# Kernel optimization log

Hardware: AMD Instinct MI355X
Metric: run time of the kernel (lower is better)

The kernel has to match this reference:

```python
import jax, jax.numpy as jnp
import numpy as np

N_WIRES = 6
DIM = 1 << N_WIRES  # 64, equals input channel dim C for amplitude encoding
HID = N_WIRES       # hidden_dim = len(ops)


def _rx(theta):
    c = jnp.cos(theta / 2).astype(jnp.complex64)
    s = jnp.sin(theta / 2).astype(jnp.complex64)
    return jnp.stack([jnp.stack([c, -1j * s]), jnp.stack([-1j * s, c])])


def _ry(theta):
    c = jnp.cos(theta / 2).astype(jnp.complex64)
    s = jnp.sin(theta / 2).astype(jnp.complex64)
    return jnp.stack([jnp.stack([c, -s]), jnp.stack([s, c])])


def _apply_1q(state, U, wire):
    # state: (N, 2, 2, ..., 2); apply 2x2 U on qubit axis wire+1
    s = jnp.moveaxis(state, wire + 1, 1)
    s = jnp.einsum('ab,nb...->na...', U, s)
    return jnp.moveaxis(s, 1, wire + 1)


def _apply_cnot(state, c, t):
    # flip target axis where control bit == 1
    s = jnp.moveaxis(state, (c + 1, t + 1), (1, 2))
    s = jnp.concatenate([s[:, :1], jnp.flip(s[:, 1:2], axis=2)], axis=1)
    return jnp.moveaxis(s, (1, 2), (c + 1, t + 1))


def _expval_z(state, wire):
    # <Z_wire> = P(bit=0) - P(bit=1)
    p = state.real ** 2 + state.imag ** 2
    p = jnp.moveaxis(p, wire + 1, 1).reshape(p.shape[0], 2, -1)
    return p[:, 0].sum(-1) - p[:, 1].sum(-1)


def _value_layer(x_flat, params, qk):
    # amplitude encoding: normalize input into state amplitudes (C == DIM)
    norm = jnp.linalg.norm(x_flat, axis=-1, keepdims=True)
    psi = (x_flat / norm).astype(jnp.complex64)
    state = psi.reshape((x_flat.shape[0],) + (2,) * N_WIRES)
    rx0, ry0, ry1 = params[0], params[1], params[2]
    for j in range(N_WIRES):
        state = _apply_1q(state, _rx(rx0[j]), j)
        state = _apply_1q(state, _ry(ry0[j]), j)
    for j in range(N_WIRES):
        state = _apply_cnot(state, j, (j + 1) % N_WIRES)
    for j in range(N_WIRES):
        state = _apply_1q(state, _ry(ry1[j]), j)
    if qk:
        z0 = _expval_z(state, 0)
        return jnp.stack([z0] * HID, axis=-1)  # qk=True replicates wire-0 <Z>
    return jnp.stack([_expval_z(state, w) for w in range(N_WIRES)], axis=-1)


def setup_inputs() -> dict:
    key = jax.random.key(0)
    k1, k2, k3, k4 = jax.random.split(key, 4)
    B, T, C = 16, 2048, DIM
    return {
        'x': jax.random.normal(k1, (B, T, C), dtype=jnp.float32),
        'params_q': jax.random.normal(k2, (3, N_WIRES), dtype=jnp.float32),
        'params_k': jax.random.normal(k3, (3, N_WIRES), dtype=jnp.float32),
        'params_v': jax.random.normal(k4, (3, N_WIRES), dtype=jnp.float32),
    }


def reference(x, params_q, params_k, params_v):
    B, T, C = x.shape
    xf = x.reshape(B * T, C)
    q = _value_layer(xf, params_q, True).reshape(B, T, HID)
    k = _value_layer(xf, params_k, True).reshape(B, T, HID)
    v = _value_layer(xf, params_v, False).reshape(B, T, HID)
    scores = jnp.einsum('btd,bsd->bts', q, k) / jnp.sqrt(jnp.float32(HID))
    attn = jax.nn.softmax(scores, axis=-1)
    return jnp.einsum('bts,bsd->btd', attn, v)
```

## Files before the change

### kernel.cpp

```cpp
#include <hip/hip_runtime.h>
#include <math.h>

#define NWIRES 6
#define DIM 64
#define NTOK 32768
#define NBATCH 16
#define TPB 2048
#define NMOM 16
#define SQRT6F 2.4494897427831781f
#define APAD 76

typedef short bf16x8 __attribute__((ext_vector_type(8)));
typedef float f32x4  __attribute__((ext_vector_type(4)));

__device__ __forceinline__ unsigned f2bfbits(float f) {
    unsigned u = __float_as_uint(f);
    return (u + 0x7FFF + ((u >> 16) & 1)) >> 16;
}
__device__ __forceinline__ float bfbits2f(unsigned b) {
    return __uint_as_float(b << 16);
}
__device__ __forceinline__ float pswap(float v) { return __shfl_xor(v, 1, 64); }

__global__ __attribute__((amdgpu_waves_per_eu(1, 4)))
__launch_bounds__(256) void qsa_sim(
        const float* __restrict__ x,
        const float* __restrict__ pq,
        const float* __restrict__ pk,
        const float* __restrict__ pv,
        float* __restrict__ zq,
        float* __restrict__ kv) {
    __shared__ unsigned short sAh[128 * APAD];
    __shared__ unsigned short sAl[128 * APAD];
    __shared__ float sTc[64], sTs[64], sP[24];
    int tid = threadIdx.x;
    int tbase = blockIdx.x * 256;
    int circ = blockIdx.y;
    const float* p = (circ == 0) ? pq : (circ == 1 ? pk : pv);

    int lane = tid & 63, wv = tid >> 6;
    int q4 = lane >> 4, c16 = lane & 15;
    float4 rw[8];
#pragma unroll
    for (int cg = 0; cg < 2; ++cg) {
        const float* xr = x + ((size_t)(tbase + wv * 64 + cg * 16 + c16)) * 64;
#pragma unroll
        for (int ks = 0; ks < 2; ++ks) {
            rw[cg * 4 + ks * 2 + 0] = *(const float4*)(xr + ks * 32 + q4 * 8);
            rw[cg * 4 + ks * 2 + 1] = *(const float4*)(xr + ks * 32 + q4 * 8 + 4);
        }
    }

    if (tid < 64) {
        int b = tid;
        float d = 0.f;
#pragma unroll
        for (int j = 0; j < 6; ++j)
            d += 0.5f * p[j] * ((b & (32 >> j)) ? -1.f : 1.f);
        float sd, cd;
        sincosf(d, &sd, &cd);
        sTc[b] = cd;
        sTs[b] = sd;
        if (b < 12) {
            float s, cc;
            sincosf(0.5f * p[6 + b], &s, &cc);
            sP[b * 2 + 0] = cc;
            sP[b * 2 + 1] = s;
        }
    }
    __syncthreads();

    {
        int ph = tid >> 7;
        int k  = (tid >> 1) & 63;
        int h  = tid & 1;
        const float* sTx = ph ? sTs : sTc;
        float v[32];
#pragma unroll
        for (int i = 0; i < 32; ++i) {
            int g = h * 32 + i;
            v[i] = (__popc(g & k) & 1) ? -sTx[g] : sTx[g];
        }
#pragma unroll
        for (int i = 0; i < 32; ++i) {
            float pv_ = pswap(v[i]);
            v[i] = h ? (pv_ - v[i]) : (v[i] + pv_);
        }
#pragma unroll
        for (int M = 16; M >= 1; M >>= 1) {
#pragma unroll
            for (int i = 0; i < 32; ++i) {
                if (i & M) continue;
                int j = i | M;
                float a = v[i], b = v[j];
                v[i] = a + b; v[j] = a - b;
            }
        }
#pragma unroll
        for (int layer = 0; layer < 2; ++layer) {
            const float* Pl = sP + layer * 12;
            {
                float c = Pl[0], ss = h ? Pl[1] : -Pl[1];
#pragma unroll
                for (int i = 0; i < 32; ++i) {
                    float pv_ = pswap(v[i]);
                    v[i] = c * v[i] + ss * pv_;
                }
            }
#pragma unroll
            for (int w = 1; w < 6; ++w) {
                int M = 32 >> w;
                float c = Pl[w * 2], s = Pl[w * 2 + 1];
#pragma unroll
                for (int i = 0; i < 32; ++i) {
                    if (i & M) continue;
                    int j = i | M;
                    float a = v[i], b = v[j];
                    v[i] = c * a - s * b;
                    v[j] = s * a + c * b;
                }
            }
            if (layer == 0) {
#pragma unroll
                for (int i = 0; i < 16; ++i) {
                    int j = i | 16;
                    float a = v[i], b = v[j];
                    v[i] = h ? b : a;
                    v[j] = h ? a : b;
                }
#pragma unroll
                for (int w = 1; w < 5; ++w) {
                    int MC = 32 >> w, MT = MC >> 1;
#pragma unroll
                    for (int i = 0; i < 32; ++i) {
                        if (!(i & MC) || (i & MT)) continue;
                        int j = i | MT;
                        float t = v[i]; v[i] = v[j]; v[j] = t;
                    }
                }
#pragma unroll
                for (int i = 1; i < 32; i += 2) v[i] = pswap(v[i]);
            }
        }
#pragma unroll
        for (int i = 0; i < 32; ++i) {
            int row = ph * 64 + h * 32 + i;
            unsigned hb = f2bfbits(v[i]);
            unsigned lb = f2bfbits(v[i] - bfbits2f(hb));
            sAh[row * APAD + k] = (unsigned short)hb;
            sAl[row * APAD + k] = (unsigned short)lb;
        }
    }
    __syncthreads();

    bf16x8 xh[2][2], xl[2][2];
#pragma unroll 1
    for (int pr = 0; pr < 2; ++pr) {
#pragma unroll
        for (int cg = 0; cg < 2; ++cg) {
#pragma unroll
            for (int ks = 0; ks < 2; ++ks) {
                float4 f0 = rw[cg * 4 + ks * 2], f1 = rw[cg * 4 + ks * 2 + 1];
                float ff[8] = {f0.x, f0.y, f0.z, f0.w, f1.x, f1.y, f1.z, f1.w};
#pragma unroll
                for (int e = 0; e < 8; ++e) {
                    unsigned hb = f2bfbits(ff[e]);
                    unsigned lb = f2bfbits(ff[e] - bfbits2f(hb));
                    xh[cg][ks][e] = (short)hb;
                    xl[cg][ks][e] = (short)lb;
                }
            }
        }
        if (pr == 0) {
#pragma unroll
            for (int cg = 0; cg < 2; ++cg) {
                const float* xr = x + ((size_t)(tbase + wv * 64 + (2 + cg) * 16 + c16)) * 64;
#pragma unroll
                for (int ks = 0; ks < 2; ++ks) {
                    rw[cg * 4 + ks * 2 + 0] = *(const float4*)(xr + ks * 32 + q4 * 8);
                    rw[cg * 4 + ks * 2 + 1] = *(const float4*)(xr + ks * 32 + q4 * 8 + 4);
                }
            }
        }

        f32x4 acc[2][8];
#pragma unroll
        for (int cg = 0; cg < 2; ++cg)
#pragma unroll
            for (int mt = 0; mt < 8; ++mt) acc[cg][mt] = (f32x4){0.f, 0.f, 0.f, 0.f};

#pragma unroll
        for (int mt = 0; mt < 8; ++mt) {
            int r = mt * 16 + c16;
#pragma unroll
            for (int ks = 0; ks < 2; ++ks) {
                const uint2* ph_ = (const uint2*)(&sAh[r * APAD + ks * 32 + q4 * 8]);
                const uint2* pl_ = (const uint2*)(&sAl[r * APAD + ks * 32 + q4 * 8]);
                union { uint2 u[2]; bf16x8 v; } ua, ub;
                ua.u[0] = ph_[0]; ua.u[1] = ph_[1];
                ub.u[0] = pl_[0]; ub.u[1] = pl_[1];
                bf16x8 ah = ua.v, al = ub.v;
#pragma unroll
                for (int cg = 0; cg < 2; ++cg) {
                    acc[cg][mt] = __builtin_amdgcn_mfma_f32_16x16x32_bf16(ah, xh[cg][ks], acc[cg][mt], 0, 0, 0);
                    acc[cg][mt] = __builtin_amdgcn_mfma_f32_16x16x32_bf16(ah, xl[cg][ks], acc[cg][mt], 0, 0, 0);
                    acc[cg][mt] = __builtin_amdgcn_mfma_f32_16x16x32_bf16(al, xh[cg][ks], acc[cg][mt], 0, 0, 0);
                }
            }
        }

#pragma unroll
        for (int cg = 0; cg < 2; ++cg) {
            float n = 0.f, s0 = 0.f, s1 = 0.f, s2 = 0.f, s3 = 0.f, s4 = 0.f, s5 = 0.f;
            float f2 = (q4 < 2) ? 1.f : 0.f;
            float f3 = (q4 & 1) ? 0.f : 1.f;
#pragma unroll
            for (int mt = 0; mt < 4; ++mt) {
#pragma unroll
                for (int rg = 0; rg < 4; ++rg) {
                    float dc = acc[cg][mt][rg];
                    float ds = acc[cg][mt + 4][rg];
                    float pp = dc * dc + ds * ds;
                    n += pp;
                    if (!(mt & 2)) s0 += pp;
                    if (!(mt & 1)) s1 += pp;
                    s2 += f2 * pp;
                    s3 += f3 * pp;
                    if (!(rg & 2)) s4 += pp;
                    if (!(rg & 1)) s5 += pp;
                }
            }
#pragma unroll
            for (int d = 16; d <= 32; d <<= 1) {
                n  += __shfl_xor(n,  d, 64);
                s0 += __shfl_xor(s0, d, 64);
                s1 += __shfl_xor(s1, d, 64);
                s2 += __shfl_xor(s2, d, 64);
                s3 += __shfl_xor(s3, d, 64);
                s4 += __shfl_xor(s4, d, 64);
                s5 += __shfl_xor(s5, d, 64);
            }
            if (q4 == 0) {
                int t = tbase + wv * 64 + (pr * 2 + cg) * 16 + c16;
                float inv = 1.0f / n;
                if (circ == 0) {
                    zq[t] = SQRT6F * (2.f * s0 - n) * inv;
                } else if (circ == 1) {
                    kv[(size_t)t * 8] = (2.f * s0 - n) * inv;
                } else {
                    float* o = kv + (size_t)t * 8;
                    o[1] = (2.f*s0 - n) * inv;
                    o[2] = (2.f*s1 - n) * inv;
                    o[3] = (2.f*s2 - n) * inv;
                    o[4] = (2.f*s3 - n) * inv;
                    o[5] = (2.f*s4 - n) * inv;
                    o[6] = (2.f*s5 - n) * inv;
                    o[7] = 0.f;
                }
            }
        }
    }
}

__global__ __attribute__((amdgpu_waves_per_eu(1, 2)))
__launch_bounds__(64) void qsa_moments_partial(
        const float* __restrict__ kv,
        float* __restrict__ mpart) {
    __shared__ float sm[64 * 113];
    int blk = blockIdx.x;
    int b = blk >> 3, c = blk & 7;
    int lane = threadIdx.x;
    float S[NMOM], H[NMOM][6];
#pragma unroll
    for (int m = 0; m < NMOM; ++m) {
        S[m] = 0.f;
#pragma unroll
        for (int w = 0; w < 6; ++w) H[m][w] = 0.f;
    }
    const float* base = kv + ((size_t)(b * TPB + c * 256)) * 8;
#pragma unroll
    for (int r = 0; r < 4; ++r) {
        const float4* e = (const float4*)(base + (size_t)(r * 64 + lane) * 8);
        float4 e0 = e[0], e1 = e[1];
        float z = e0.x;
        float v0 = e0.y, v1 = e0.z, v2 = e0.w, v3 = e1.x, v4 = e1.y, v5 = e1.z;
        float pw = 1.f;
#pragma unroll
        for (int m = 0; m < NMOM; ++m) {
            S[m] += pw;
            H[m][0] += pw * v0; H[m][1] += pw * v1; H[m][2] += pw * v2;
            H[m][3] += pw * v3; H[m][4] += pw * v4; H[m][5] += pw * v5;
            pw *= z;
        }
    }
    float* row = sm + lane * 113;
#pragma unroll
    for (int m = 0; m < NMOM; ++m) {
        row[m * 7 + 0] = S[m];
        row[m * 7 + 1] = H[m][0]; row[m * 7 + 2] = H[m][1];
        row[m * 7 + 3] = H[m][2]; row[m * 7 + 4] = H[m][3];
        row[m * 7 + 5] = H[m][4]; row[m * 7 + 6] = H[m][5];
    }
    __syncthreads();
#pragma unroll
    for (int vbase = 0; vbase < 2; ++vbase) {
        int v = vbase * 64 + lane;
        if (v < 112) {
            float s = 0.f;
#pragma unroll
            for (int r = 0; r < 64; ++r) s += sm[r * 113 + v];
            mpart[(size_t)blk * 112 + v] = s;
        }
    }
}

__global__ __launch_bounds__(256) void qsa_eval(
        const float* __restrict__ zq,
        const float* __restrict__ mpart,
        float* __restrict__ out) {
    __shared__ float sm[112];
    int bk = blockIdx.x;
    int b = bk >> 3;
    int tid = threadIdx.x;
    if (tid < 112) {
        float s = 0.f;
#pragma unroll
        for (int c = 0; c < 8; ++c) s += mpart[(size_t)(b * 8 + c) * 112 + tid];
        sm[tid] = s;
    }
    __syncthreads();

    int t = bk * 256 + tid;
    float a = zq[t];
    float den = 0.f, o0 = 0.f, o1 = 0.f, o2 = 0.f, o3 = 0.f, o4 = 0.f, o5 = 0.f;
    float pw = 1.f;
#pragma unroll
    for (int m = 0; m < NMOM; ++m) {
        const float* mm = sm + m * 7;
        den += pw * mm[0];
        o0 += pw * mm[1]; o1 += pw * mm[2]; o2 += pw * mm[3];
        o3 += pw * mm[4]; o4 += pw * mm[5]; o5 += pw * mm[6];
        pw *= a * (1.0f / (m + 1));
    }
    float inv = 1.0f / den;
    float* o = out + (size_t)t * 6;
    float2* o2p = (float2*)o;
    o2p[0] = make_float2(o0 * inv, o1 * inv);
    o2p[1] = make_float2(o2 * inv, o3 * inv);
    o2p[2] = make_float2(o4 * inv, o5 * inv);
}

extern "C" void kernel_launch(void* const* d_in, const int* in_sizes, int n_in,
                              void* d_out, int out_size, void* d_ws, size_t ws_size,
                              hipStream_t stream) {
    const float* x  = (const float*)d_in[0];
    const float* pq = (const float*)d_in[1];
    const float* pk = (const float*)d_in[2];
    const float* pv = (const float*)d_in[3];
    float* w = (float*)d_ws;
    float* zq    = w;
    float* kv    = zq + NTOK;
    float* mpart = kv + NTOK * 8;
    float* out   = (float*)d_out;

    qsa_sim<<<dim3(NTOK / 256, 3), 256, 0, stream>>>(x, pq, pk, pv, zq, kv);
    qsa_moments_partial<<<NBATCH * 8, 64, 0, stream>>>(kv, mpart);
    qsa_eval<<<NTOK / 256, 256, 0, stream>>>(zq, mpart, out);
}
```

Measured before the change: 88.48 us.

## Fuse moment reduction into simulation kernel and share x tiles across K/V

The separate moments kernel and the global kv intermediate buffer are removed. Each block of the second grid row now builds unitaries for both the K and V circuits, evaluates both on the same x registers, and stages z and v expectations in LDS. It then computes the per-block power moments there and writes mpart directly. This saves one kernel launch, a global write and read of the kv buffer, and one of the three passes over x. In exchange the K/V blocks carry twice the work of the Q blocks, and LDS use per block roughly doubles, which may lower occupancy.

```diff
diff --git a/kernel.cpp b/kernel.cpp
--- a/kernel.cpp
+++ b/kernel.cpp
@@ -9,6 +9,7 @@
 #define NMOM 16
 #define SQRT6F 2.4494897427831781f
 #define APAD 76
+#define ZP 260
 
 typedef short bf16x8 __attribute__((ext_vector_type(8)));
 typedef float f32x4  __attribute__((ext_vector_type(4)));
@@ -22,35 +23,10 @@
 }
 __device__ __forceinline__ float pswap(float v) { return __shfl_xor(v, 1, 64); }
 
-__global__ __attribute__((amdgpu_waves_per_eu(1, 4)))
-__launch_bounds__(256) void qsa_sim(
-        const float* __restrict__ x,
-        const float* __restrict__ pq,
-        const float* __restrict__ pk,
-        const float* __restrict__ pv,
-        float* __restrict__ zq,
-        float* __restrict__ kv) {
-    __shared__ unsigned short sAh[128 * APAD];
-    __shared__ unsigned short sAl[128 * APAD];
-    __shared__ float sTc[64], sTs[64], sP[24];
-    int tid = threadIdx.x;
-    int tbase = blockIdx.x * 256;
-    int circ = blockIdx.y;
-    const float* p = (circ == 0) ? pq : (circ == 1 ? pk : pv);
-
-    int lane = tid & 63, wv = tid >> 6;
-    int q4 = lane >> 4, c16 = lane & 15;
-    float4 rw[8];
-#pragma unroll
-    for (int cg = 0; cg < 2; ++cg) {
-        const float* xr = x + ((size_t)(tbase + wv * 64 + cg * 16 + c16)) * 64;
-#pragma unroll
-        for (int ks = 0; ks < 2; ++ks) {
-            rw[cg * 4 + ks * 2 + 0] = *(const float4*)(xr + ks * 32 + q4 * 8);
-            rw[cg * 4 + ks * 2 + 1] = *(const float4*)(xr + ks * 32 + q4 * 8 + 4);
-        }
-    }
-
+
+__device__ __forceinline__ void build_A(const float* __restrict__ p,
+        unsigned short* sAh, unsigned short* sAl,
+        float* sTc, float* sTs, float* sP, int tid) {
     if (tid < 64) {
         int b = tid;
         float d = 0.f;
@@ -152,6 +128,48 @@
         }
     }
     __syncthreads();
+}
+
+__global__ __attribute__((amdgpu_waves_per_eu(1, 4)))
+__launch_bounds__(256) void qsa_sim(
+        const float* __restrict__ x,
+        const float* __restrict__ pq,
+        const float* __restrict__ pk,
+        const float* __restrict__ pv,
+        float* __restrict__ zq,
+        float* __restrict__ mpart) {
+    __shared__ __align__(16) unsigned short sAbuf[4 * 128 * APAD];
+    __shared__ float sTc[64], sTs[64], sP[24];
+    __shared__ float zT[256];
+    __shared__ __align__(16) float vT[6 * ZP];
+    __shared__ float sred[224];
+    int tid = threadIdx.x;
+    int tbase = blockIdx.x * 256;
+    int circ = blockIdx.y;
+
+    int lane = tid & 63, wv = tid >> 6;
+    int q4 = lane >> 4, c16 = lane & 15;
+    float4 rw[8];
+#pragma unroll
+    for (int cg = 0; cg < 2; ++cg) {
+        const float* xr = x + ((size_t)(tbase + wv * 64 + cg * 16 + c16)) * 64;
+#pragma unroll
+        for (int ks = 0; ks < 2; ++ks) {
+            rw[cg * 4 + ks * 2 + 0] = *(const float4*)(xr + ks * 32 + q4 * 8);
+            rw[cg * 4 + ks * 2 + 1] = *(const float4*)(xr + ks * 32 + q4 * 8 + 4);
+        }
+    }
+
+    int ncirc;
+    if (circ == 0) {
+        build_A(pq, sAbuf, sAbuf + 128 * APAD, sTc, sTs, sP, tid);
+        ncirc = 1;
+    } else {
+        build_A(pk, sAbuf, sAbuf + 128 * APAD, sTc, sTs, sP, tid);
+        build_A(pv, sAbuf + 2 * 128 * APAD, sAbuf + 3 * 128 * APAD,
+                sTc, sTs, sP, tid);
+        ncirc = 2;
+    }
 
     bf16x8 xh[2][2], xl[2][2];
 #pragma unroll 1
@@ -183,133 +201,125 @@
             }
         }
 
-        f32x4 acc[2][8];
-#pragma unroll
-        for (int cg = 0; cg < 2; ++cg)
-#pragma unroll
-            for (int mt = 0; mt < 8; ++mt) acc[cg][mt] = (f32x4){0.f, 0.f, 0.f, 0.f};
-
-#pragma unroll
-        for (int mt = 0; mt < 8; ++mt) {
-            int r = mt * 16 + c16;
-#pragma unroll
-            for (int ks = 0; ks < 2; ++ks) {
-                const uint2* ph_ = (const uint2*)(&sAh[r * APAD + ks * 32 + q4 * 8]);
-                const uint2* pl_ = (const uint2*)(&sAl[r * APAD + ks * 32 + q4 * 8]);
-                union { uint2 u[2]; bf16x8 v; } ua, ub;
-                ua.u[0] = ph_[0]; ua.u[1] = ph_[1];
-                ub.u[0] = pl_[0]; ub.u[1] = pl_[1];
-                bf16x8 ah = ua.v, al = ub.v;
-#pragma unroll
-                for (int cg = 0; cg < 2; ++cg) {
-                    acc[cg][mt] = __builtin_amdgcn_mfma_f32_16x16x32_bf16(ah, xh[cg][ks], acc[cg][mt], 0, 0, 0);
-                    acc[cg][mt] = __builtin_amdgcn_mfma_f32_16x16x32_bf16(ah, xl[cg][ks], acc[cg][mt], 0, 0, 0);
-                    acc[cg][mt] = __builtin_amdgcn_mfma_f32_16x16x32_bf16(al, xh[cg][ks], acc[cg][mt], 0, 0, 0);
-                }
-            }
-        }
-
-#pragma unroll
-        for (int cg = 0; cg < 2; ++cg) {
-            float n = 0.f, s0 = 0.f, s1 = 0.f, s2 = 0.f, s3 = 0.f, s4 = 0.f, s5 = 0.f;
-            float f2 = (q4 < 2) ? 1.f : 0.f;
-            float f3 = (q4 & 1) ? 0.f : 1.f;
-#pragma unroll
-            for (int mt = 0; mt < 4; ++mt) {
-#pragma unroll
-                for (int rg = 0; rg < 4; ++rg) {
-                    float dc = acc[cg][mt][rg];
-                    float ds = acc[cg][mt + 4][rg];
-                    float pp = dc * dc + ds * ds;
-                    n += pp;
-                    if (!(mt & 2)) s0 += pp;
-                    if (!(mt & 1)) s1 += pp;
-                    s2 += f2 * pp;
-                    s3 += f3 * pp;
-                    if (!(rg & 2)) s4 += pp;
-                    if (!(rg & 1)) s5 += pp;
-                }
-            }
-#pragma unroll
-            for (int d = 16; d <= 32; d <<= 1) {
-                n  += __shfl_xor(n,  d, 64);
-                s0 += __shfl_xor(s0, d, 64);
-                s1 += __shfl_xor(s1, d, 64);
-                s2 += __shfl_xor(s2, d, 64);
-                s3 += __shfl_xor(s3, d, 64);
-                s4 += __shfl_xor(s4, d, 64);
-                s5 += __shfl_xor(s5, d, 64);
-            }
-            if (q4 == 0) {
-                int t = tbase + wv * 64 + (pr * 2 + cg) * 16 + c16;
-                float inv = 1.0f / n;
-                if (circ == 0) {
-                    zq[t] = SQRT6F * (2.f * s0 - n) * inv;
-                } else if (circ == 1) {
-                    kv[(size_t)t * 8] = (2.f * s0 - n) * inv;
-                } else {
-                    float* o = kv + (size_t)t * 8;
-                    o[1] = (2.f*s0 - n) * inv;
-                    o[2] = (2.f*s1 - n) * inv;
-                    o[3] = (2.f*s2 - n) * inv;
-                    o[4] = (2.f*s3 - n) * inv;
-                    o[5] = (2.f*s4 - n) * inv;
-                    o[6] = (2.f*s5 - n) * inv;
-                    o[7] = 0.f;
-                }
-            }
-        }
-    }
-}
-
-__global__ __attribute__((amdgpu_waves_per_eu(1, 2)))
-__launch_bounds__(64) void qsa_moments_partial(
-        const float* __restrict__ kv,
-        float* __restrict__ mpart) {
-    __shared__ float sm[64 * 113];
-    int blk = blockIdx.x;
-    int b = blk >> 3, c = blk & 7;
-    int lane = threadIdx.x;
-    float S[NMOM], H[NMOM][6];
-#pragma unroll
-    for (int m = 0; m < NMOM; ++m) {
-        S[m] = 0.f;
-#pragma unroll
-        for (int w = 0; w < 6; ++w) H[m][w] = 0.f;
-    }
-    const float* base = kv + ((size_t)(b * TPB + c * 256)) * 8;
-#pragma unroll
-    for (int r = 0; r < 4; ++r) {
-        const float4* e = (const float4*)(base + (size_t)(r * 64 + lane) * 8);
-        float4 e0 = e[0], e1 = e[1];
-        float z = e0.x;
-        float v0 = e0.y, v1 = e0.z, v2 = e0.w, v3 = e1.x, v4 = e1.y, v5 = e1.z;
-        float pw = 1.f;
-#pragma unroll
-        for (int m = 0; m < NMOM; ++m) {
-            S[m] += pw;
-            H[m][0] += pw * v0; H[m][1] += pw * v1; H[m][2] += pw * v2;
-            H[m][3] += pw * v3; H[m][4] += pw * v4; H[m][5] += pw * v5;
-            pw *= z;
-        }
-    }
-    float* row = sm + lane * 113;
-#pragma unroll
-    for (int m = 0; m < NMOM; ++m) {
-        row[m * 7 + 0] = S[m];
-        row[m * 7 + 1] = H[m][0]; row[m * 7 + 2] = H[m][1];
-        row[m * 7 + 3] = H[m][2]; row[m * 7 + 4] = H[m][3];
-        row[m * 7 + 5] = H[m][4]; row[m * 7 + 6] = H[m][5];
-    }
-    __syncthreads();
-#pragma unroll
-    for (int vbase = 0; vbase < 2; ++vbase) {
-        int v = vbase * 64 + lane;
-        if (v < 112) {
-            float s = 0.f;
-#pragma unroll
-            for (int r = 0; r < 64; ++r) s += sm[r * 113 + v];
-            mpart[(size_t)blk * 112 + v] = s;
+#pragma unroll 1
+        for (int cc = 0; cc < ncirc; ++cc) {
+            const unsigned short* Ah = sAbuf + cc * (2 * 128 * APAD);
+            const unsigned short* Al = Ah + 128 * APAD;
+
+            f32x4 acc[2][8];
+#pragma unroll
+            for (int cg = 0; cg < 2; ++cg)
+#pragma unroll
+                for (int mt = 0; mt < 8; ++mt) acc[cg][mt] = (f32x4){0.f, 0.f, 0.f, 0.f};
+
+#pragma unroll
+            for (int mt = 0; mt < 8; ++mt) {
+                int r = mt * 16 + c16;
+#pragma unroll
+                for (int ks = 0; ks < 2; ++ks) {
+                    const uint2* ph_ = (const uint2*)(&Ah[r * APAD + ks * 32 + q4 * 8]);
+                    const uint2* pl_ = (const uint2*)(&Al[r * APAD + ks * 32 + q4 * 8]);
+                    union { uint2 u[2]; bf16x8 v; } ua, ub;
+                    ua.u[0] = ph_[0]; ua.u[1] = ph_[1];
+                    ub.u[0] = pl_[0]; ub.u[1] = pl_[1];
+                    bf16x8 ah = ua.v, al = ub.v;
+#pragma unroll
+                    for (int cg = 0; cg < 2; ++cg) {
+                        acc[cg][mt] = __builtin_amdgcn_mfma_f32_16x16x32_bf16(ah, xh[cg][ks], acc[cg][mt], 0, 0, 0);
+                        acc[cg][mt] = __builtin_amdgcn_mfma_f32_16x16x32_bf16(ah, xl[cg][ks], acc[cg][mt], 0, 0, 0);
+                        acc[cg][mt] = __builtin_amdgcn_mfma_f32_16x16x32_bf16(al, xh[cg][ks], acc[cg][mt], 0, 0, 0);
+                    }
+                }
+            }
+
+#pragma unroll
+            for (int cg = 0; cg < 2; ++cg) {
+                float n = 0.f, s0 = 0.f, s1 = 0.f, s2 = 0.f, s3 = 0.f, s4 = 0.f, s5 = 0.f;
+                float f2 = (q4 < 2) ? 1.f : 0.f;
+                float f3 = (q4 & 1) ? 0.f : 1.f;
+#pragma unroll
+                for (int mt = 0; mt < 4; ++mt) {
+#pragma unroll
+                    for (int rg = 0; rg < 4; ++rg) {
+                        float dc = acc[cg][mt][rg];
+                        float ds = acc[cg][mt + 4][rg];
+                        float pp = dc * dc + ds * ds;
+                        n += pp;
+                        if (!(mt & 2)) s0 += pp;
+                        if (!(mt & 1)) s1 += pp;
+                        s2 += f2 * pp;
+                        s3 += f3 * pp;
+                        if (!(rg & 2)) s4 += pp;
+                        if (!(rg & 1)) s5 += pp;
+                    }
+                }
+#pragma unroll
+                for (int d = 16; d <= 32; d <<= 1) {
+                    n  += __shfl_xor(n,  d, 64);
+                    s0 += __shfl_xor(s0, d, 64);
+                    s1 += __shfl_xor(s1, d, 64);
+                    s2 += __shfl_xor(s2, d, 64);
+                    s3 += __shfl_xor(s3, d, 64);
+                    s4 += __shfl_xor(s4, d, 64);
+                    s5 += __shfl_xor(s5, d, 64);
+                }
+                if (q4 == 0) {
+                    int tl = wv * 64 + (pr * 2 + cg) * 16 + c16;
+                    float inv = 1.0f / n;
+                    if (circ == 0) {
+                        zq[tbase + tl] = SQRT6F * (2.f * s0 - n) * inv;
+                    } else if (cc == 0) {
+                        zT[tl] = (2.f * s0 - n) * inv;
+                    } else {
+                        vT[0 * ZP + tl] = (2.f * s0 - n) * inv;
+                        vT[1 * ZP + tl] = (2.f * s1 - n) * inv;
+                        vT[2 * ZP + tl] = (2.f * s2 - n) * inv;
+                        vT[3 * ZP + tl] = (2.f * s3 - n) * inv;
+                        vT[4 * ZP + tl] = (2.f * s4 - n) * inv;
+                        vT[5 * ZP + tl] = (2.f * s5 - n) * inv;
+                    }
+                }
+            }
+        }
+    }
+
+    if (circ == 1) {
+        __syncthreads();
+        float* zpow = (float*)sAbuf;
+        {
+            float z = zT[tid];
+            float pw = 1.f;
+#pragma unroll
+            for (int m = 0; m < NMOM; ++m) { zpow[m * ZP + tid] = pw; pw *= z; }
+        }
+        __syncthreads();
+        if (tid < 224) {
+            int h = (tid >= 112) ? 1 : 0;
+            int j = tid - h * 112;
+            int m = j / 7, w = j - m * 7;
+            const float4* zp = (const float4*)&zpow[m * ZP + h * 128];
+            float a = 0.f;
+            if (w == 6) {
+#pragma unroll
+                for (int k = 0; k < 32; ++k) {
+                    float4 a4 = zp[k];
+                    a += a4.x + a4.y + a4.z + a4.w;
+                }
+            } else {
+                const float4* vp = (const float4*)&vT[w * ZP + h * 128];
+#pragma unroll
+                for (int k = 0; k < 32; ++k) {
+                    float4 a4 = zp[k], b4 = vp[k];
+                    a += a4.x * b4.x + a4.y * b4.y + a4.z * b4.z + a4.w * b4.w;
+                }
+            }
+            sred[tid] = a;
+        }
+        __syncthreads();
+        if (tid < 112) {
+            int m = tid / 7, w = tid - m * 7;
+            int idx = m * 7 + ((w == 6) ? 0 : (w + 1));
+            mpart[(size_t)blockIdx.x * 112 + idx] = sred[tid] + sred[tid + 112];
         }
     }
 }
@@ -359,11 +369,9 @@
     const float* pv = (const float*)d_in[3];
     float* w = (float*)d_ws;
     float* zq    = w;
-    float* kv    = zq + NTOK;
-    float* mpart = kv + NTOK * 8;
+    float* mpart = zq + NTOK;
     float* out   = (float*)d_out;
 
-    qsa_sim<<<dim3(NTOK / 256, 3), 256, 0, stream>>>(x, pq, pk, pv, zq, kv);
-    qsa_moments_partial<<<NBATCH * 8, 64, 0, stream>>>(kv, mpart);
+    qsa_sim<<<dim3(NTOK / 256, 2), 256, 0, stream>>>(x, pq, pk, pv, zq, mpart);
     qsa_eval<<<NTOK / 256, 256, 0, stream>>>(zq, mpart, out);
 }
```

After: 85.07 us (median of 2 runs). 1.04x faster.
